# Kernel tuning notes

Measured on AMD Instinct MI355X. Metric: run time of the kernel, lower is better.

## Reference

```python
import jax, jax.numpy as jnp
import numpy as np

IN_DIM = 64  # channels; theta/phi -> C//8, g -> C//2


def _maxpool2x2(t):
    # t: [B, c, H, W] -> [B, c, H//2, W//2]
    B, c, H, W = t.shape
    return t.reshape(B, c, H // 2, 2, W // 2, 2).max(axis=(3, 5))


def setup_inputs() -> dict:
    key = jax.random.key(0)
    ks = jax.random.split(key, 6)
    C = IN_DIM
    x = jax.random.normal(ks[0], (16, C, 64, 64), dtype=jnp.float32)
    # 1x1 convs stored as [out, in] matrices (kernel is 1x1, no bias)
    w_theta = jax.random.normal(ks[1], (C // 8, C), dtype=jnp.float32) * (1.0 / np.sqrt(C))
    w_phi = jax.random.normal(ks[2], (C // 8, C), dtype=jnp.float32) * (1.0 / np.sqrt(C))
    w_g = jax.random.normal(ks[3], (C // 2, C), dtype=jnp.float32) * (1.0 / np.sqrt(C))
    w_o = jax.random.normal(ks[4], (C, C // 2), dtype=jnp.float32) * (1.0 / np.sqrt(C // 2))
    gamma = jax.random.normal(ks[5], (), dtype=jnp.float32)  # torch inits to 0; nonzero for testing
    return {"x": x, "w_theta": w_theta, "w_phi": w_phi, "w_g": w_g, "w_o": w_o, "gamma": gamma}


def reference(x, w_theta, w_phi, w_g, w_o, gamma):
    B, C, H, W = x.shape
    # 1x1 conv projections (pointwise channel matmuls)
    theta = jnp.einsum('oc,bchw->bohw', w_theta, x).reshape(B, C // 8, H * W)
    phi = _maxpool2x2(jnp.einsum('oc,bchw->bohw', w_phi, x)).reshape(B, C // 8, H * W // 4)
    g = _maxpool2x2(jnp.einsum('oc,bchw->bohw', w_g, x)).reshape(B, C // 2, H * W // 4)
    # attention: [B, HW, HW/4]
    beta = jax.nn.softmax(jnp.einsum('bcn,bcm->bnm', theta, phi), axis=-1)
    # aggregate values: g @ beta^T -> [B, C//2, HW]
    o = jnp.einsum('bcm,bnm->bcn', g, beta).reshape(B, C // 2, H, W)
    o = jnp.einsum('oc,bchw->bohw', w_o, o)
    return gamma * o + x
```

## Files before the change

### kernel.cpp

```cpp
#include <hip/hip_runtime.h>

typedef _Float16 half4v __attribute__((ext_vector_type(4)));
typedef _Float16 h2     __attribute__((ext_vector_type(2)));
typedef float    float4v __attribute__((ext_vector_type(4)));

#define BB 16
#define CC 64
#define NN 4096
#define MM 1024
#define LN256 5.545177444479562f

static __device__ __forceinline__ float4v mfma16(half4v a, half4v b, float4v c) {
    return __builtin_amdgcn_mfma_f32_16x16x16f16(a, b, c, 0, 0, 0);
}

__device__ __forceinline__ unsigned pk2(float a, float b) {
    union { _Float16 h[2]; unsigned u; } cv;
    cv.h[0] = (_Float16)a; cv.h[1] = (_Float16)b;
    return cv.u;
}
__device__ __forceinline__ h2 ash2(unsigned u) {
    union { unsigned u; h2 h; } c; c.u = u; return c.h;
}
__device__ __forceinline__ h2 hmax2(h2 a, h2 b) {
    h2 r;
    r.x = (a.x > b.x) ? a.x : b.x;
    r.y = (a.y > b.y) ? a.y : b.y;
    return r;
}
__device__ __forceinline__ h2 shfl_xor_h2(h2 v, int m) {
    union { h2 h; int i; } c; c.h = v; c.i = __shfl_xor(c.i, m);
    return c.h;
}

__global__ __launch_bounds__(128, 4) void proj_kernel(
    const float* __restrict__ x,
    const float* __restrict__ w_th,
    const float* __restrict__ w_ph,
    const float* __restrict__ w_g,
    _Float16* __restrict__ theta,
    _Float16* __restrict__ phi,
    _Float16* __restrict__ gT)
{
    __shared__ __align__(16) float wlds[64 * 16];
    unsigned* wl2 = (unsigned*)wlds;

    const int b   = blockIdx.y;
    const int blk = blockIdx.x;
    const int z   = blockIdx.z;
    const int t   = threadIdx.x;

    if (z == 0) {
        for (int i = t; i < 1024; i += 128) {
            int c = i >> 4, o = i & 15;
            wlds[i] = (o < 8) ? w_th[o * 64 + c] : w_ph[(o - 8) * 64 + c];
        }
    } else {
        for (int i = t; i < 1024; i += 128) {
            int c = i >> 4, o2 = i & 15;
            wl2[i] = pk2(w_g[(2 * o2) * 64 + c], w_g[(2 * o2 + 1) * 64 + c]);
        }
    }
    __syncthreads();

    const float2* x2 = (const float2*)(x + (size_t)b * CC * NN);
    const int p2 = blk * 128 + t;
    const int l = t & 63, w = t >> 6;
    const int m = (blk * 2 + w) * 32 + (l & 31);

    if (z == 0) {
        float th0[8], th1[8], ph0[8], ph1[8];
#pragma unroll
        for (int i = 0; i < 8; i++) { th0[i]=th1[i]=ph0[i]=ph1[i]=0.f; }
#pragma unroll 4
        for (int c = 0; c < 64; c++) {
            float2 xv = x2[c * (NN / 2) + p2];
            const float4* w4 = (const float4*)&wlds[c * 16];
            float4 wv[4];
#pragma unroll
            for (int j = 0; j < 4; j++) wv[j] = w4[j];
            const float* wf = (const float*)wv;
#pragma unroll
            for (int o = 0; o < 8; o++) {
                th0[o] = fmaf(wf[o], xv.x, th0[o]);
                th1[o] = fmaf(wf[o], xv.y, th1[o]);
                ph0[o] = fmaf(wf[8 + o], xv.x, ph0[o]);
                ph1[o] = fmaf(wf[8 + o], xv.y, ph1[o]);
            }
        }
        uint4* tw = (uint4*)(theta + ((size_t)b * NN + 2 * p2) * 8);
        tw[0] = make_uint4(pk2(th0[0],th0[1]), pk2(th0[2],th0[3]),
                           pk2(th0[4],th0[5]), pk2(th0[6],th0[7]));
        tw[1] = make_uint4(pk2(th1[0],th1[1]), pk2(th1[2],th1[3]),
                           pk2(th1[4],th1[5]), pk2(th1[6],th1[7]));
        float phm[8];
#pragma unroll
        for (int i = 0; i < 8; i++) phm[i] = fmaxf(ph0[i], ph1[i]);
#pragma unroll
        for (int i = 0; i < 8; i++) phm[i] = fmaxf(phm[i], __shfl_xor(phm[i], 32));
        if (l < 32) {
            uint4* pw = (uint4*)(phi + ((size_t)b * MM + m) * 8);
            pw[0] = make_uint4(pk2(phm[0],phm[1]), pk2(phm[2],phm[3]),
                               pk2(phm[4],phm[5]), pk2(phm[6],phm[7]));
        }
    } else {
        h2 ga[16], gb[16];
#pragma unroll
        for (int i = 0; i < 16; i++) { ga[i] = (h2)0; gb[i] = (h2)0; }
#pragma unroll 4
        for (int c = 0; c < 64; c++) {
            float2 xv = x2[c * (NN / 2) + p2];
            const uint4* w4 = (const uint4*)&wl2[c * 16];
            uint4 q0 = w4[0], q1 = w4[1], q2 = w4[2], q3 = w4[3];
            unsigned wv[16] = {q0.x,q0.y,q0.z,q0.w, q1.x,q1.y,q1.z,q1.w,
                               q2.x,q2.y,q2.z,q2.w, q3.x,q3.y,q3.z,q3.w};
            _Float16 hx = (_Float16)xv.x, hy = (_Float16)xv.y;
            h2 xa; xa.x = hx; xa.y = hx;
            h2 xb; xb.x = hy; xb.y = hy;
#pragma unroll
            for (int k = 0; k < 16; k++) {
                ga[k] = __builtin_elementwise_fma(ash2(wv[k]), xa, ga[k]);
                gb[k] = __builtin_elementwise_fma(ash2(wv[k]), xb, gb[k]);
            }
        }
        h2 gm[16];
#pragma unroll
        for (int k = 0; k < 16; k++) gm[k] = hmax2(ga[k], gb[k]);
#pragma unroll
        for (int k = 0; k < 16; k++) gm[k] = hmax2(gm[k], shfl_xor_h2(gm[k], 32));
        const int k0 = (l < 32) ? 0 : 8;
        _Float16* gp = gT + ((size_t)b * 32 + 2 * k0) * MM + m;
#pragma unroll
        for (int k = 0; k < 8; k++) {
            h2 v = gm[k0 + k];
            gp[(size_t)(2 * k) * MM]     = v.x;
            gp[(size_t)(2 * k + 1) * MM] = v.y;
        }
    }
}

__global__ __launch_bounds__(256, 4) void attn_kernel(
    const _Float16* __restrict__ theta,
    const _Float16* __restrict__ phi,
    const _Float16* __restrict__ gT,
    const float* __restrict__ w_o,
    const float* __restrict__ gamma_p,
    const float* __restrict__ x,
    float* __restrict__ out)
{
    __shared__ __align__(16) _Float16 phl[MM * 8];
    __shared__ __align__(16) _Float16 gl[2][32 * 136];

    const int b    = blockIdx.y;
    const int t    = threadIdx.x;
    const int wave = t >> 6;
    const int lane = t & 63;
    const int col  = lane & 15;
    const int q    = lane >> 4;
    const int nbase = blockIdx.x * 64 + wave * 16;

    const float4v zero4 = {0.f, 0.f, 0.f, 0.f};
    const half4v zeroh = {0, 0, 0, 0};

    {
        const float4* src = (const float4*)(phi + (size_t)b * MM * 8);
        float4* dst = (float4*)phl;
#pragma unroll
        for (int i = 0; i < 4; i++) dst[t + i * 256] = src[t + i * 256];
    }

    half4v thB = zeroh;
    if (q < 2)
        thB = *(const half4v*)(theta + ((size_t)b * NN + nbase + col) * 8 + q * 4);

    half4v onesA = zeroh;
    if (col == 0) {
        onesA[0] = (_Float16)1; onesA[1] = (_Float16)1;
        onesA[2] = (_Float16)1; onesA[3] = (_Float16)1;
    }

    __syncthreads();

    float mx = -1e30f;
#pragma unroll 4
    for (int mt = 0; mt < 64; mt++) {
        half4v af = zeroh;
        if (q < 2)
            af = *(const half4v*)&phl[(mt * 16 + col) * 8 + q * 4];
        float4v S = mfma16(af, thB, zero4);
        mx = fmaxf(mx, fmaxf(fmaxf(S.x, S.y), fmaxf(S.z, S.w)));
    }
    mx = fmaxf(mx, __shfl_xor(mx, 16));
    mx = fmaxf(mx, __shfl_xor(mx, 32));
    const float shift = mx - LN256;

    float4v acc0 = zero4, acc1 = zero4, accd = zero4;

    const int sc_c = t >> 3, sc_s = (t & 7) * 16;
    {
        const _Float16* src = gT + ((size_t)b * 32 + sc_c) * MM + sc_s;
        *(float4*)&gl[0][sc_c * 136 + sc_s]     = *(const float4*)src;
        *(float4*)&gl[0][sc_c * 136 + sc_s + 8] = *(const float4*)(src + 8);
    }
    __syncthreads();

    for (int c8 = 0; c8 < 8; c8++) {
        const int cur = c8 & 1;
        if (c8 < 7) {
            const _Float16* src =
                gT + ((size_t)b * 32 + sc_c) * MM + (c8 + 1) * 128 + sc_s;
            *(float4*)&gl[1 - cur][sc_c * 136 + sc_s]     = *(const float4*)src;
            *(float4*)&gl[1 - cur][sc_c * 136 + sc_s + 8] = *(const float4*)(src + 8);
        }

#pragma unroll 2
        for (int mt = 0; mt < 8; mt++) {
            half4v af = zeroh;
            if (q < 2)
                af = *(const half4v*)&phl[(c8 * 128 + mt * 16 + col) * 8 + q * 4];
            float4v S = mfma16(af, thB, zero4);
            half4v P;
            P[0] = (_Float16)__expf(S.x - shift);
            P[1] = (_Float16)__expf(S.y - shift);
            P[2] = (_Float16)__expf(S.z - shift);
            P[3] = (_Float16)__expf(S.w - shift);
            half4v ag0 = *(const half4v*)&gl[cur][col * 136 + mt * 16 + q * 4];
            half4v ag1 = *(const half4v*)&gl[cur][(col + 16) * 136 + mt * 16 + q * 4];
            acc0 = mfma16(ag0, P, acc0);
            acc1 = mfma16(ag1, P, acc1);
            accd = mfma16(onesA, P, accd);
        }
        __syncthreads();
    }

    float dv = __shfl(accd.x, col);
    float sc = gamma_p[0] / dv;

    half4v B0, B1;
    B0[0] = (_Float16)(acc0.x * sc); B0[1] = (_Float16)(acc0.y * sc);
    B0[2] = (_Float16)(acc0.z * sc); B0[3] = (_Float16)(acc0.w * sc);
    B1[0] = (_Float16)(acc1.x * sc); B1[1] = (_Float16)(acc1.y * sc);
    B1[2] = (_Float16)(acc1.z * sc); B1[3] = (_Float16)(acc1.w * sc);

#pragma unroll
    for (int ct = 0; ct < 4; ct++) {
        const float* wp = w_o + (size_t)(ct * 16 + col) * 32 + q * 4;
        float4 w0 = *(const float4*)wp;
        float4 w1 = *(const float4*)(wp + 16);
        half4v wa, wb;
        wa[0] = (_Float16)w0.x; wa[1] = (_Float16)w0.y;
        wa[2] = (_Float16)w0.z; wa[3] = (_Float16)w0.w;
        wb[0] = (_Float16)w1.x; wb[1] = (_Float16)w1.y;
        wb[2] = (_Float16)w1.z; wb[3] = (_Float16)w1.w;
        float4v D = mfma16(wa, B0, zero4);
        D = mfma16(wb, B1, D);
#pragma unroll
        for (int r = 0; r < 4; r++) {
            int co = ct * 16 + q * 4 + r;
            size_t idx = ((size_t)b * CC + co) * NN + nbase + col;
            out[idx] = D[r] + x[idx];
        }
    }
}

extern "C" void kernel_launch(void* const* d_in, const int* in_sizes, int n_in,
                              void* d_out, int out_size, void* d_ws, size_t ws_size,
                              hipStream_t stream) {
    const float* x       = (const float*)d_in[0];
    const float* w_theta = (const float*)d_in[1];
    const float* w_phi   = (const float*)d_in[2];
    const float* w_g     = (const float*)d_in[3];
    const float* w_o     = (const float*)d_in[4];
    const float* gamma   = (const float*)d_in[5];
    float* out = (float*)d_out;

    _Float16* theta_ws = (_Float16*)d_ws;
    _Float16* phi_ws   = theta_ws + (size_t)BB * NN * 8;
    _Float16* gT_ws    = phi_ws   + (size_t)BB * MM * 8;

    proj_kernel<<<dim3(16, BB, 2), 128, 0, stream>>>(
        x, w_theta, w_phi, w_g, theta_ws, phi_ws, gT_ws);

    attn_kernel<<<dim3(NN / 64, BB), 256, 0, stream>>>(
        theta_ws, phi_ws, gT_ws, w_o, gamma, x, out);
}
```

Baseline: 119.0 us.

## Stage full g tile in swizzled LDS with 512-thread blocks

The attention kernel now uses 512-thread blocks covering 128 query rows each. Each block loads the entire g^T slice for its batch (32x1024 halves) into LDS once, replacing the double-buffered 128-column chunks and their per-chunk barriers. The global loads for phi and g are issued up front and written to LDS after the max pass, so their latency overlaps it. XOR-swizzled addressing is added for the phi and g LDS layouts to avoid bank conflicts. In exchange, LDS use per block rises to about 80KB, which limits blocks per CU, and each thread holds ten extra float4 registers.

```diff
diff --git a/kernel.cpp b/kernel.cpp
--- a/kernel.cpp
+++ b/kernel.cpp
@@ -31,6 +31,10 @@
 __device__ __forceinline__ h2 shfl_xor_h2(h2 v, int m) {
     union { h2 h; int i; } c; c.h = v; c.i = __shfl_xor(c.i, m);
     return c.h;
+}
+
+__device__ __forceinline__ int gl_off(int c, int m) {
+    return (c * 2048 + m * 2) ^ (((c ^ (m >> 6)) & 15) << 3);
 }
 
 __global__ __launch_bounds__(128, 4) void proj_kernel(
@@ -139,7 +143,7 @@
     }
 }
 
-__global__ __launch_bounds__(256, 4) void attn_kernel(
+__global__ __launch_bounds__(512, 4) void attn_kernel(
     const _Float16* __restrict__ theta,
     const _Float16* __restrict__ phi,
     const _Float16* __restrict__ gT,
@@ -149,7 +153,7 @@
     float* __restrict__ out)
 {
     __shared__ __align__(16) _Float16 phl[MM * 8];
-    __shared__ __align__(16) _Float16 gl[2][32 * 136];
+    __shared__ __align__(16) _Float16 gl[32 * MM];
 
     const int b    = blockIdx.y;
     const int t    = threadIdx.x;
@@ -157,17 +161,17 @@
     const int lane = t & 63;
     const int col  = lane & 15;
     const int q    = lane >> 4;
-    const int nbase = blockIdx.x * 64 + wave * 16;
+    const int nbase = blockIdx.x * 128 + wave * 16;
 
     const float4v zero4 = {0.f, 0.f, 0.f, 0.f};
     const half4v zeroh = {0, 0, 0, 0};
 
-    {
-        const float4* src = (const float4*)(phi + (size_t)b * MM * 8);
-        float4* dst = (float4*)phl;
-#pragma unroll
-        for (int i = 0; i < 4; i++) dst[t + i * 256] = src[t + i * 256];
-    }
+    const float4* ph4 = (const float4*)(phi + (size_t)b * MM * 8);
+    const float4* gt4 = (const float4*)(gT + (size_t)b * 32 * MM);
+    float4 pr0 = ph4[t], pr1 = ph4[t + 512];
+    float4 gr[8];
+#pragma unroll
+    for (int j = 0; j < 8; j++) gr[j] = gt4[t + j * 512];
 
     half4v thB = zeroh;
     if (q < 2)
@@ -179,14 +183,25 @@
         onesA[2] = (_Float16)1; onesA[3] = (_Float16)1;
     }
 
+    char* phb = (char*)phl;
+    {
+        int m = t;
+        *(float2*)(phb + ((m * 16)     ^ (m & 8))) = *(const float2*)&pr0;
+        *(float2*)(phb + ((m * 16 + 8) ^ (m & 8))) = *((const float2*)&pr0 + 1);
+        m = t + 512;
+        *(float2*)(phb + ((m * 16)     ^ (m & 8))) = *(const float2*)&pr1;
+        *(float2*)(phb + ((m * 16 + 8) ^ (m & 8))) = *((const float2*)&pr1 + 1);
+    }
     __syncthreads();
 
     float mx = -1e30f;
 #pragma unroll 4
     for (int mt = 0; mt < 64; mt++) {
         half4v af = zeroh;
-        if (q < 2)
-            af = *(const half4v*)&phl[(mt * 16 + col) * 8 + q * 4];
+        if (q < 2) {
+            int m = mt * 16 + col;
+            af = *(const half4v*)(phb + ((m * 16 + q * 8) ^ (m & 8)));
+        }
         float4v S = mfma16(af, thB, zero4);
         mx = fmaxf(mx, fmaxf(fmaxf(S.x, S.y), fmaxf(S.z, S.w)));
     }
@@ -194,43 +209,37 @@
     mx = fmaxf(mx, __shfl_xor(mx, 32));
     const float shift = mx - LN256;
 
+    char* glb = (char*)gl;
+#pragma unroll
+    for (int j = 0; j < 8; j++) {
+        int idx4 = t + j * 512;
+        int c = idx4 >> 7;
+        int m = (idx4 & 127) * 8;
+        *(float2*)(glb + gl_off(c, m))     = *(const float2*)&gr[j];
+        *(float2*)(glb + gl_off(c, m + 4)) = *((const float2*)&gr[j] + 1);
+    }
+    __syncthreads();
+
     float4v acc0 = zero4, acc1 = zero4, accd = zero4;
-
-    const int sc_c = t >> 3, sc_s = (t & 7) * 16;
-    {
-        const _Float16* src = gT + ((size_t)b * 32 + sc_c) * MM + sc_s;
-        *(float4*)&gl[0][sc_c * 136 + sc_s]     = *(const float4*)src;
-        *(float4*)&gl[0][sc_c * 136 + sc_s + 8] = *(const float4*)(src + 8);
-    }
-    __syncthreads();
-
-    for (int c8 = 0; c8 < 8; c8++) {
-        const int cur = c8 & 1;
-        if (c8 < 7) {
-            const _Float16* src =
-                gT + ((size_t)b * 32 + sc_c) * MM + (c8 + 1) * 128 + sc_s;
-            *(float4*)&gl[1 - cur][sc_c * 136 + sc_s]     = *(const float4*)src;
-            *(float4*)&gl[1 - cur][sc_c * 136 + sc_s + 8] = *(const float4*)(src + 8);
-        }
-
-#pragma unroll 2
-        for (int mt = 0; mt < 8; mt++) {
-            half4v af = zeroh;
-            if (q < 2)
-                af = *(const half4v*)&phl[(c8 * 128 + mt * 16 + col) * 8 + q * 4];
-            float4v S = mfma16(af, thB, zero4);
-            half4v P;
-            P[0] = (_Float16)__expf(S.x - shift);
-            P[1] = (_Float16)__expf(S.y - shift);
-            P[2] = (_Float16)__expf(S.z - shift);
-            P[3] = (_Float16)__expf(S.w - shift);
-            half4v ag0 = *(const half4v*)&gl[cur][col * 136 + mt * 16 + q * 4];
-            half4v ag1 = *(const half4v*)&gl[cur][(col + 16) * 136 + mt * 16 + q * 4];
-            acc0 = mfma16(ag0, P, acc0);
-            acc1 = mfma16(ag1, P, acc1);
-            accd = mfma16(onesA, P, accd);
-        }
-        __syncthreads();
+#pragma unroll 4
+    for (int mt = 0; mt < 64; mt++) {
+        half4v af = zeroh;
+        if (q < 2) {
+            int m = mt * 16 + col;
+            af = *(const half4v*)(phb + ((m * 16 + q * 8) ^ (m & 8)));
+        }
+        float4v S = mfma16(af, thB, zero4);
+        half4v P;
+        P[0] = (_Float16)__expf(S.x - shift);
+        P[1] = (_Float16)__expf(S.y - shift);
+        P[2] = (_Float16)__expf(S.z - shift);
+        P[3] = (_Float16)__expf(S.w - shift);
+        const int m0 = mt * 16 + q * 4;
+        half4v ag0 = *(const half4v*)(glb + gl_off(col,      m0));
+        half4v ag1 = *(const half4v*)(glb + gl_off(col + 16, m0));
+        acc0 = mfma16(ag0, P, acc0);
+        acc1 = mfma16(ag1, P, acc1);
+        accd = mfma16(onesA, P, accd);
     }
 
     float dv = __shfl(accd.x, col);
@@ -281,6 +290,6 @@
     proj_kernel<<<dim3(16, BB, 2), 128, 0, stream>>>(
         x, w_theta, w_phi, w_g, theta_ws, phi_ws, gT_ws);
 
-    attn_kernel<<<dim3(NN / 64, BB), 256, 0, stream>>>(
+    attn_kernel<<<dim3(NN / 128, BB), 512, 0, stream>>>(
         theta_ws, phi_ws, gT_ws, w_o, gamma, x, out);
 }
```

New measurement: 120.8 us. No clear change (+1.5%).
